# Performance work log

Hardware: AMD Instinct MI355X
Metric: run time of the kernel (lower is better)

Reference implementation:

```python
import jax, jax.numpy as jnp
import numpy as np

# Static config (matches init_kwargs)
B, C, H, W = 8, 256, 128, 128
K = 8            # window size per spatial dim
S = K // 2       # shift size
HEADS = 8
E = 256          # embedding_dim
HEAD_DIM = E // HEADS
HID = 3 * C      # mlp hidden
L = K * K        # tokens per window
NW = (H // K) * (W // K)  # windows per image
EPS = 1e-5


def _shift_mask_np():
    # Standard Swin shifted-window attention mask: True = masked.
    img = np.zeros((H, W), dtype=np.int32)
    cnt = 0
    for hs in (slice(0, -K), slice(-K, -S), slice(-S, None)):
        for ws in (slice(0, -K), slice(-K, -S), slice(-S, None)):
            img[hs, ws] = cnt
            cnt += 1
    ids = img.reshape(H // K, K, W // K, K).transpose(0, 2, 1, 3).reshape(NW, L)
    return ids[:, :, None] != ids[:, None, :]  # (NW, L, L) bool

SHIFT_MASK = jnp.asarray(_shift_mask_np())  # (NW, L, L)


def _rpe_index_np():
    coords = np.stack(np.meshgrid(np.arange(K), np.arange(K), indexing='ij'), -1).reshape(L, 2)
    rel = coords[:, None, :] - coords[None, :, :] + (K - 1)  # (L, L, 2) in [0, 2K-2]
    return rel[..., 0] * (2 * K - 1) + rel[..., 1]  # (L, L)

RPE_IDX = jnp.asarray(_rpe_index_np())  # (L, L) int


def window_partition(x):
    # (B, C, H, W) -> (B, NW, L, C)
    x = x.reshape(B, C, H // K, K, W // K, K)
    return x.transpose(0, 2, 4, 3, 5, 1).reshape(B, NW, L, C)


def window_unpartition(x):
    # (B, NW, L, C) -> (B, C, H, W)
    x = x.reshape(B, H // K, W // K, K, K, C)
    return x.transpose(0, 5, 1, 3, 2, 4).reshape(B, C, H, W)


def layer_norm(x, g, b):
    m = jnp.mean(x, axis=-1, keepdims=True)
    v = jnp.mean(jnp.square(x - m), axis=-1, keepdims=True)
    return (x - m) * jax.lax.rsqrt(v + EPS) * g + b


def setup_inputs() -> dict:
    key = jax.random.key(0)
    ks = jax.random.split(key, 12)
    sc = 0.02
    return {
        'query': jax.random.normal(ks[0], (B, C, H, W), jnp.float32),
        'w_q': jax.random.normal(ks[1], (E, C), jnp.float32) * sc,
        'b_q': jnp.zeros((E,), jnp.float32),
        'w_k': jax.random.normal(ks[2], (E, C), jnp.float32) * sc,
        'b_k': jnp.zeros((E,), jnp.float32),
        'w_v': jax.random.normal(ks[3], (E, C), jnp.float32) * sc,
        'b_v': jnp.zeros((E,), jnp.float32),
        'w_proj': jax.random.normal(ks[4], (C, E), jnp.float32) * sc,
        'b_proj': jnp.zeros((C,), jnp.float32),
        'gamma_attn': jnp.ones((C,), jnp.float32),
        'beta_attn': jnp.zeros((C,), jnp.float32),
        'w1': jax.random.normal(ks[5], (HID, C), jnp.float32) * sc,
        'b1': jnp.zeros((HID,), jnp.float32),
        'w2': jax.random.normal(ks[6], (C, HID), jnp.float32) * sc,
        'b2': jnp.zeros((C,), jnp.float32),
        'gamma_mlp': jnp.ones((C,), jnp.float32),
        'beta_mlp': jnp.zeros((C,), jnp.float32),
        'rpe_table': jax.random.normal(ks[7], ((2 * K - 1) ** 2, HEADS), jnp.float32) * sc,
    }


def reference(query, w_q, b_q, w_k, b_k, w_v, b_v, w_proj, b_proj,
              gamma_attn, beta_attn, w1, b1, w2, b2, gamma_mlp, beta_mlp,
              rpe_table) -> jnp.ndarray:
    # cyclic shift (shifted=True)
    xs = jnp.roll(query, (-S, -S), axis=(2, 3))
    xw = window_partition(xs)  # (B, NW, L, C)

    # windowed multi-head attention with relative positional bias
    q = (jnp.einsum('bwlc,ec->bwle', xw, w_q) + b_q).reshape(B, NW, L, HEADS, HEAD_DIM)
    k = (jnp.einsum('bwlc,ec->bwle', xw, w_k) + b_k).reshape(B, NW, L, HEADS, HEAD_DIM)
    v = (jnp.einsum('bwlc,ec->bwle', xw, w_v) + b_v).reshape(B, NW, L, HEADS, HEAD_DIM)
    scale = HEAD_DIM ** -0.5
    scores = jnp.einsum('bwqhd,bwkhd->bwhqk', q, k) * scale  # (B, NW, H, L, L)
    bias = rpe_table[RPE_IDX].transpose(2, 0, 1)  # (HEADS, L, L)
    scores = scores + bias
    scores = jnp.where(SHIFT_MASK[None, :, None, :, :], jnp.float32(-1e9), scores)
    attn = jax.nn.softmax(scores, axis=-1)
    ctx = jnp.einsum('bwhqk,bwkhd->bwqhd', attn, v).reshape(B, NW, L, E)
    attn_out = jnp.einsum('bwle,ce->bwlc', ctx, w_proj) + b_proj

    # post-attention norm + residual (dropout/droppath inactive in eval)
    x = layer_norm(attn_out, gamma_attn, beta_attn) + xw

    # MLP (GELU) + norm + residual
    h = jax.nn.gelu(jnp.einsum('bwlc,hc->bwlh', x, w1) + b1)
    mlp_out = jnp.einsum('bwlh,ch->bwlc', h, w2) + b2
    x = layer_norm(mlp_out, gamma_mlp, beta_mlp) + x

    out = window_unpartition(x)  # (B, C, H, W)
    return jnp.roll(out, (S, S), axis=(2, 3))
```

## Files before the change

### kernel.cpp

```cpp
#include <hip/hip_runtime.h>
#include <hip/hip_bf16.h>

typedef __attribute__((ext_vector_type(8))) __bf16 bf16x8;
typedef __attribute__((ext_vector_type(4))) float f32x4;
typedef __hip_bfloat16 bf16_t;

#define MFMA(a, b, c) __builtin_amdgcn_mfma_f32_16x16x32_bf16((a), (b), (c), 0, 0, 0)

constexpr int XS = 264;
constexpr int CS = 72;
constexpr int XBYTES = 64 * XS * 2;
constexpr int QC_OFF = XBYTES;
constexpr int KC_OFF = QC_OFF + 64 * CS * 2;
constexpr int VC_OFF = KC_OFF + 64 * CS * 2;
constexpr int SCR_OFF = XBYTES + XBYTES;
constexpr int RPE_OFF = SCR_OFF + 64 * 8 * 4;
constexpr int SMEM_TOTAL = RPE_OFF + 225 * 8 * 4;

constexpr size_t O_WQ = 0;
constexpr size_t O_BQ = O_WQ + 65536;
constexpr size_t O_WK = O_BQ + 256;
constexpr size_t O_BK = O_WK + 65536;
constexpr size_t O_WV = O_BK + 256;
constexpr size_t O_BV = O_WV + 65536;
constexpr size_t O_WP = O_BV + 256;
constexpr size_t O_BP = O_WP + 65536;
constexpr size_t O_GA = O_BP + 256;
constexpr size_t O_BA = O_GA + 256;
constexpr size_t O_W1 = O_BA + 256;
constexpr size_t O_B1 = O_W1 + 196608;
constexpr size_t O_W2 = O_B1 + 768;
constexpr size_t O_B2 = O_W2 + 196608;
constexpr size_t O_GM = O_B2 + 256;
constexpr size_t O_BM = O_GM + 256;
constexpr size_t O_RPE = O_BM + 256;
constexpr size_t W_TOTAL = O_RPE + 1800;

__device__ __forceinline__ float red16(float v) {
    v += __shfl_xor(v, 1);
    v += __shfl_xor(v, 2);
    v += __shfl_xor(v, 4);
    v += __shfl_xor(v, 8);
    return v;
}
__device__ __forceinline__ unsigned short bfbits(float x) {
    bf16_t b = __float2bfloat16(x);
    unsigned short u;
    __builtin_memcpy(&u, &b, 2);
    return u;
}
__device__ __forceinline__ ushort4 pack4(float a, float b, float c, float d) {
    ushort4 u;
    u.x = bfbits(a); u.y = bfbits(b); u.z = bfbits(c); u.w = bfbits(d);
    return u;
}

template <typename T>
__device__ __forceinline__ bf16x8 ldfrag(const T* p) {
    if constexpr (sizeof(T) == 4) {
        const float4* q = reinterpret_cast<const float4*>(p);
        float4 a = q[0], b = q[1];
        bf16x8 r;
        r[0] = static_cast<__bf16>(a.x); r[1] = static_cast<__bf16>(a.y);
        r[2] = static_cast<__bf16>(a.z); r[3] = static_cast<__bf16>(a.w);
        r[4] = static_cast<__bf16>(b.x); r[5] = static_cast<__bf16>(b.y);
        r[6] = static_cast<__bf16>(b.z); r[7] = static_cast<__bf16>(b.w);
        return r;
    } else {
        return *reinterpret_cast<const bf16x8*>(p);
    }
}
template <typename T>
__device__ __forceinline__ float ld1(const T* p) {
    if constexpr (sizeof(T) == 4) return *reinterpret_cast<const float*>(p);
    else return __bfloat162float(*reinterpret_cast<const bf16_t*>(p));
}

template <typename T, typename WT>
__device__ void swin_body(
    const T* __restrict__ qin,
    const WT* __restrict__ wq, const WT* __restrict__ bq,
    const WT* __restrict__ wk, const WT* __restrict__ bk,
    const WT* __restrict__ wv, const WT* __restrict__ bv,
    const WT* __restrict__ wp, const WT* __restrict__ bp,
    const WT* __restrict__ ga, const WT* __restrict__ ba,
    const WT* __restrict__ w1, const WT* __restrict__ b1,
    const WT* __restrict__ w2, const WT* __restrict__ b2,
    const WT* __restrict__ gm, const WT* __restrict__ bm,
    const WT* __restrict__ rpe,
    float* __restrict__ outp, char* sm)
{
    bf16_t* xb = reinterpret_cast<bf16_t*>(sm);
    unsigned short* xbs = reinterpret_cast<unsigned short*>(sm);
    bf16_t* qcp = reinterpret_cast<bf16_t*>(sm + QC_OFF);
    bf16_t* kcp = reinterpret_cast<bf16_t*>(sm + KC_OFF);
    bf16_t* vcp = reinterpret_cast<bf16_t*>(sm + VC_OFF);
    float*  scr = reinterpret_cast<float*>(sm + SCR_OFF);
    float*  rpl = reinterpret_cast<float*>(sm + RPE_OFF);
    bf16_t* hb  = reinterpret_cast<bf16_t*>(sm + XBYTES);

    const int tid  = threadIdx.x;
    const int wave = tid >> 6;
    const int lane = tid & 63;
    const int quad = lane >> 4;
    const int l15  = lane & 15;
    const int h32  = (wave & 1) * 32;
    const int rw   = (wave >> 1) * 32;
    const int colbase = wave * 64;

    const int sw = ((blockIdx.x & 7) << 8) | (blockIdx.x >> 3);
    const int bi = sw >> 8;
    const int wl = sw & 255;
    const int wh = wl >> 4, ww = wl & 15;

    const T* qbase = qin + (size_t)bi * (256 * 128 * 128);

    for (int u = tid; u < 4096; u += 256) {
        int ch = u >> 4, r = (u >> 1) & 7, hf = u & 1;
        int hs = (wh * 8 + r + 4) & 127;
        int ws = (ww * 8 + hf * 4 + 4) & 127;
        int t0 = r * 8 + hf * 4;
        if constexpr (sizeof(T) == 4) {
            float4 px = *reinterpret_cast<const float4*>(
                reinterpret_cast<const float*>(qbase) + ch * 16384 + hs * 128 + ws);
            xb[(t0 + 0) * XS + ch] = __float2bfloat16(px.x);
            xb[(t0 + 1) * XS + ch] = __float2bfloat16(px.y);
            xb[(t0 + 2) * XS + ch] = __float2bfloat16(px.z);
            xb[(t0 + 3) * XS + ch] = __float2bfloat16(px.w);
        } else {
            ushort4 px = *reinterpret_cast<const ushort4*>(
                reinterpret_cast<const unsigned short*>(qbase) + ch * 16384 + hs * 128 + ws);
            xbs[(t0 + 0) * XS + ch] = px.x;
            xbs[(t0 + 1) * XS + ch] = px.y;
            xbs[(t0 + 2) * XS + ch] = px.z;
            xbs[(t0 + 3) * XS + ch] = px.w;
        }
    }
    for (int u = tid; u < 1800; u += 256)
        rpl[(u & 7) * 225 + (u >> 3)] = ld1(rpe + u);
    __syncthreads();

    const f32x4 zero = {0.f, 0.f, 0.f, 0.f};

    const bool wh15 = (wh == 15), ww15 = (ww == 15);
    int ridx_[2][4][4];
    unsigned int msk_bits = 0;
    for (int mt = 0; mt < 2; ++mt) {
        int qt = rw + mt * 16 + l15;
        int qr = qt >> 3, qc = qt & 7;
        int qid = (wh15 ? (qr < 4 ? 1 : 2) : 0) * 3 + (ww15 ? (qc < 4 ? 1 : 2) : 0);
        for (int nt = 0; nt < 4; ++nt)
            for (int i = 0; i < 4; ++i) {
                int kt = nt * 16 + quad * 4 + i;
                int kr = kt >> 3, kc = kt & 7;
                int kid = (wh15 ? (kr < 4 ? 1 : 2) : 0) * 3 + (ww15 ? (kc < 4 ? 1 : 2) : 0);
                ridx_[mt][nt][i] = (qr - kr + 7) * 15 + (qc - kc + 7);
                if (qid != kid) msk_bits |= 1u << (mt * 16 + nt * 4 + i);
            }
    }

    f32x4 pacc[4][4];
    for (int mt = 0; mt < 4; ++mt) for (int nt = 0; nt < 4; ++nt) pacc[mt][nt] = zero;

    #pragma unroll 1
    for (int p = 0; p < 4; ++p) {
        const int ecb = p * 64;

        bf16x8 wpa[2][4];
        for (int kbi = 0; kbi < 2; ++kbi)
            for (int nt = 0; nt < 4; ++nt)
                wpa[kbi][nt] = ldfrag<WT>(
                    wp + (size_t)(colbase + nt * 16 + l15) * 256 + ecb + kbi * 32 + quad * 8);

        {
            f32x4 qa[4], ka[4], va[4];
            for (int mt = 0; mt < 4; ++mt) { qa[mt] = zero; ka[mt] = zero; va[mt] = zero; }
            const size_t wrow = (size_t)(ecb + wave * 16 + l15) * 256;
            bf16x8 bqf = ldfrag<WT>(wq + wrow + quad * 8);
            bf16x8 bkf = ldfrag<WT>(wk + wrow + quad * 8);
            bf16x8 bvf = ldfrag<WT>(wv + wrow + quad * 8);
            #pragma unroll
            for (int kb = 0; kb < 256; kb += 32) {
                const int kbn = (kb + 32) & 255;
                bf16x8 nqf = ldfrag<WT>(wq + wrow + kbn + quad * 8);
                bf16x8 nkf = ldfrag<WT>(wk + wrow + kbn + quad * 8);
                bf16x8 nvf = ldfrag<WT>(wv + wrow + kbn + quad * 8);
                bf16x8 xf[4];
                for (int mt = 0; mt < 4; ++mt)
                    xf[mt] = *reinterpret_cast<const bf16x8*>(
                        xb + (mt * 16 + l15) * XS + kb + quad * 8);
                __builtin_amdgcn_s_setprio(1);
                for (int mt = 0; mt < 4; ++mt) {
                    qa[mt] = MFMA(bqf, xf[mt], qa[mt]);
                    ka[mt] = MFMA(bkf, xf[mt], ka[mt]);
                    va[mt] = MFMA(xf[mt], bvf, va[mt]);
                }
                __builtin_amdgcn_s_setprio(0);
                bqf = nqf; bkf = nkf; bvf = nvf;
            }
            float bq4[4], bk4[4];
            for (int i = 0; i < 4; ++i) {
                bq4[i] = ld1(bq + ecb + wave * 16 + quad * 4 + i);
                bk4[i] = ld1(bk + ecb + wave * 16 + quad * 4 + i);
            }
            float bbv = ld1(bv + ecb + wave * 16 + l15);
            const float SC = 0.17677669529663687f;
            for (int mt = 0; mt < 4; ++mt) {
                *reinterpret_cast<ushort4*>(qcp + (mt * 16 + l15) * CS + wave * 16 + quad * 4) =
                    pack4((qa[mt][0] + bq4[0]) * SC, (qa[mt][1] + bq4[1]) * SC,
                          (qa[mt][2] + bq4[2]) * SC, (qa[mt][3] + bq4[3]) * SC);
                *reinterpret_cast<ushort4*>(kcp + (mt * 16 + l15) * CS + wave * 16 + quad * 4) =
                    pack4(ka[mt][0] + bk4[0], ka[mt][1] + bk4[1],
                          ka[mt][2] + bk4[2], ka[mt][3] + bk4[3]);
                *reinterpret_cast<ushort4*>(vcp + (wave * 16 + l15) * CS + mt * 16 + quad * 4) =
                    pack4(va[mt][0] + bbv, va[mt][1] + bbv,
                          va[mt][2] + bbv, va[mt][3] + bbv);
            }
        }
        __syncthreads();

        f32x4 sacc[2][4];
        {
            bf16x8 bf_q[2], af_k[4];
            for (int mt = 0; mt < 2; ++mt)
                bf_q[mt] = *reinterpret_cast<const bf16x8*>(
                    qcp + (rw + mt * 16 + l15) * CS + h32 + quad * 8);
            for (int nt = 0; nt < 4; ++nt)
                af_k[nt] = *reinterpret_cast<const bf16x8*>(
                    kcp + (nt * 16 + l15) * CS + h32 + quad * 8);
            __builtin_amdgcn_s_setprio(1);
            for (int mt = 0; mt < 2; ++mt)
                for (int nt = 0; nt < 4; ++nt)
                    sacc[mt][nt] = MFMA(af_k[nt], bf_q[mt], zero);
            __builtin_amdgcn_s_setprio(0);
        }
        __syncthreads();

        const float* rph = rpl + (2 * p + (wave & 1)) * 225;
        bf16_t* preg = (wave & 1) ? kcp : qcp;
        for (int mt = 0; mt < 2; ++mt) {
            for (int nt = 0; nt < 4; ++nt)
                for (int i = 0; i < 4; ++i) {
                    float s = sacc[mt][nt][i];
                    s += rph[ridx_[mt][nt][i]];
                    if (msk_bits & (1u << (mt * 16 + nt * 4 + i))) s = -1e9f;
                    sacc[mt][nt][i] = s;
                }
            float m = sacc[mt][0][0];
            for (int nt = 0; nt < 4; ++nt)
                for (int i = 0; i < 4; ++i) m = fmaxf(m, sacc[mt][nt][i]);
            m = fmaxf(m, __shfl_xor(m, 16));
            m = fmaxf(m, __shfl_xor(m, 32));
            float ssum = 0.f;
            for (int nt = 0; nt < 4; ++nt)
                for (int i = 0; i < 4; ++i) {
                    float e = __expf(sacc[mt][nt][i] - m);
                    sacc[mt][nt][i] = e;
                    ssum += e;
                }
            ssum += __shfl_xor(ssum, 16);
            ssum += __shfl_xor(ssum, 32);
            float inv = 1.0f / ssum;
            for (int nt = 0; nt < 4; ++nt)
                *reinterpret_cast<ushort4*>(
                    preg + (rw + mt * 16 + l15) * CS + nt * 16 + quad * 4) =
                    pack4(sacc[mt][nt][0] * inv, sacc[mt][nt][1] * inv,
                          sacc[mt][nt][2] * inv, sacc[mt][nt][3] * inv);
        }

        f32x4 cacc[2][2];
        for (int mt = 0; mt < 2; ++mt) for (int n2 = 0; n2 < 2; ++n2) cacc[mt][n2] = zero;
        for (int kb = 0; kb < 64; kb += 32) {
            bf16x8 bf_p[2], af_v[2];
            for (int mt = 0; mt < 2; ++mt)
                bf_p[mt] = *reinterpret_cast<const bf16x8*>(
                    preg + (rw + mt * 16 + l15) * CS + kb + quad * 8);
            for (int n2 = 0; n2 < 2; ++n2)
                af_v[n2] = *reinterpret_cast<const bf16x8*>(
                    vcp + (h32 + n2 * 16 + l15) * CS + kb + quad * 8);
            __builtin_amdgcn_s_setprio(1);
            for (int mt = 0; mt < 2; ++mt)
                for (int n2 = 0; n2 < 2; ++n2)
                    cacc[mt][n2] = MFMA(af_v[n2], bf_p[mt], cacc[mt][n2]);
            __builtin_amdgcn_s_setprio(0);
        }
        for (int mt = 0; mt < 2; ++mt)
            for (int n2 = 0; n2 < 2; ++n2)
                *reinterpret_cast<ushort4*>(
                    preg + (rw + mt * 16 + l15) * CS + n2 * 16 + quad * 4) =
                    pack4(cacc[mt][n2][0], cacc[mt][n2][1],
                          cacc[mt][n2][2], cacc[mt][n2][3]);
        __syncthreads();

        for (int kbi = 0; kbi < 2; ++kbi) {
            const bf16_t* creg = kbi ? kcp : qcp;
            bf16x8 af[4];
            for (int mt = 0; mt < 4; ++mt)
                af[mt] = *reinterpret_cast<const bf16x8*>(
                    creg + (mt * 16 + l15) * CS + quad * 8);
            __builtin_amdgcn_s_setprio(1);
            for (int mt = 0; mt < 4; ++mt)
                for (int nt = 0; nt < 4; ++nt)
                    pacc[mt][nt] = MFMA(af[mt], wpa[kbi][nt], pacc[mt][nt]);
            __builtin_amdgcn_s_setprio(0);
        }
        __syncthreads();
    }

    auto layernorm_resid = [&](f32x4 (&acc)[4][4], const WT* gamma, const WT* beta) {
        for (int mt = 0; mt < 4; ++mt)
            for (int rg = 0; rg < 4; ++rg) {
                float s = 0.f, sq = 0.f;
                for (int nt = 0; nt < 4; ++nt) {
                    float v = acc[mt][nt][rg];
                    s += v;
                    sq += v * v;
                }
                s = red16(s);
                sq = red16(sq);
                if (l15 == 0) {
                    int tok = mt * 16 + quad * 4 + rg;
                    scr[tok * 8 + wave * 2 + 0] = s;
                    scr[tok * 8 + wave * 2 + 1] = sq;
                }
            }
        __syncthreads();
        for (int mt = 0; mt < 4; ++mt)
            for (int rg = 0; rg < 4; ++rg) {
                int tok = mt * 16 + quad * 4 + rg;
                float S = 0.f, SQ = 0.f;
                for (int w_ = 0; w_ < 4; ++w_) {
                    S += scr[tok * 8 + w_ * 2 + 0];
                    SQ += scr[tok * 8 + w_ * 2 + 1];
                }
                float mean = S * (1.f / 256.f);
                float var = fmaxf(SQ * (1.f / 256.f) - mean * mean, 0.f);
                float rstd = rsqrtf(var + 1e-5f);
                for (int nt = 0; nt < 4; ++nt) {
                    int c = colbase + nt * 16 + l15;
                    float g = ld1(gamma + c);
                    float b_ = ld1(beta + c);
                    float res = __bfloat162float(xb[tok * XS + c]);
                    float o = (acc[mt][nt][rg] - mean) * rstd * g + b_ + res;
                    xb[tok * XS + c] = __float2bfloat16(o);
                }
            }
        __syncthreads();
    };

    {
        for (int nt = 0; nt < 4; ++nt) {
            float bb = ld1(bp + colbase + nt * 16 + l15);
            for (int mt = 0; mt < 4; ++mt)
                for (int rg = 0; rg < 4; ++rg) pacc[mt][nt][rg] += bb;
        }
        layernorm_resid(pacc, ga, ba);
    }

    {
        f32x4 oacc[4][4];
        for (int mt = 0; mt < 4; ++mt) for (int nt = 0; nt < 4; ++nt) oacc[mt][nt] = zero;
        for (int hc = 0; hc < 3; ++hc) {
            f32x4 hacc[4][4];
            for (int nt = 0; nt < 4; ++nt) for (int mt = 0; mt < 4; ++mt) hacc[nt][mt] = zero;
            {
                bf16x8 wf[4], nwf[4];
                for (int nt = 0; nt < 4; ++nt)
                    wf[nt] = ldfrag<WT>(
                        w1 + (size_t)(hc * 256 + colbase + nt * 16 + l15) * 256 + quad * 8);
                #pragma unroll
                for (int kb = 0; kb < 256; kb += 32) {
                    const int kbn = (kb + 32) & 255;
                    for (int nt = 0; nt < 4; ++nt)
                        nwf[nt] = ldfrag<WT>(
                            w1 + (size_t)(hc * 256 + colbase + nt * 16 + l15) * 256 + kbn + quad * 8);
                    bf16x8 xf[4];
                    for (int mt = 0; mt < 4; ++mt)
                        xf[mt] = *reinterpret_cast<const bf16x8*>(
                            xb + (mt * 16 + l15) * XS + kb + quad * 8);
                    __builtin_amdgcn_s_setprio(1);
                    for (int nt = 0; nt < 4; ++nt)
                        for (int mt = 0; mt < 4; ++mt)
                            hacc[nt][mt] = MFMA(wf[nt], xf[mt], hacc[nt][mt]);
                    __builtin_amdgcn_s_setprio(0);
                    for (int nt = 0; nt < 4; ++nt) wf[nt] = nwf[nt];
                }
            }
            for (int nt = 0; nt < 4; ++nt) {
                float b4[4];
                for (int i = 0; i < 4; ++i)
                    b4[i] = ld1(b1 + hc * 256 + colbase + nt * 16 + quad * 4 + i);
                for (int mt = 0; mt < 4; ++mt) {
                    float g4[4];
                    for (int i = 0; i < 4; ++i) {
                        float x = hacc[nt][mt][i] + b4[i];
                        float u = 0.7978845608f * (x + 0.044715f * x * x * x);
                        float t = 1.f - 2.f / (1.f + __expf(2.f * u));
                        g4[i] = 0.5f * x * (1.f + t);
                    }
                    *reinterpret_cast<ushort4*>(
                        hb + (mt * 16 + l15) * XS + colbase + nt * 16 + quad * 4) =
                        pack4(g4[0], g4[1], g4[2], g4[3]);
                }
            }
            __syncthreads();
            {
                bf16x8 bfr[4], nbfr[4];
                for (int nt = 0; nt < 4; ++nt)
                    bfr[nt] = ldfrag<WT>(
                        w2 + (size_t)(colbase + nt * 16 + l15) * 768 + hc * 256 + quad * 8);
                #pragma unroll
                for (int kb = 0; kb < 256; kb += 32) {
                    const int kbn = (kb + 32) & 255;
                    for (int nt = 0; nt < 4; ++nt)
                        nbfr[nt] = ldfrag<WT>(
                            w2 + (size_t)(colbase + nt * 16 + l15) * 768 + hc * 256 + kbn + quad * 8);
                    bf16x8 af[4];
                    for (int mt = 0; mt < 4; ++mt)
                        af[mt] = *reinterpret_cast<const bf16x8*>(
                            hb + (mt * 16 + l15) * XS + kb + quad * 8);
                    __builtin_amdgcn_s_setprio(1);
                    for (int mt = 0; mt < 4; ++mt)
                        for (int nt = 0; nt < 4; ++nt)
                            oacc[mt][nt] = MFMA(af[mt], bfr[nt], oacc[mt][nt]);
                    __builtin_amdgcn_s_setprio(0);
                    for (int nt = 0; nt < 4; ++nt) bfr[nt] = nbfr[nt];
                }
            }
            __syncthreads();
        }
        for (int nt = 0; nt < 4; ++nt) {
            float bb = ld1(b2 + colbase + nt * 16 + l15);
            for (int mt = 0; mt < 4; ++mt)
                for (int rg = 0; rg < 4; ++rg) oacc[mt][nt][rg] += bb;
        }
        layernorm_resid(oacc, gm, bm);
    }

    for (int u = tid; u < 4096; u += 256) {
        int ch = u >> 4, r = (u >> 1) & 7, hf = u & 1;
        int hs = (wh * 8 + r + 4) & 127;
        int ws = (ww * 8 + hf * 4 + 4) & 127;
        int t0 = r * 8 + hf * 4;
        float4 px;
        px.x = __bfloat162float(xb[(t0 + 0) * XS + ch]);
        px.y = __bfloat162float(xb[(t0 + 1) * XS + ch]);
        px.z = __bfloat162float(xb[(t0 + 2) * XS + ch]);
        px.w = __bfloat162float(xb[(t0 + 3) * XS + ch]);
        *reinterpret_cast<float4*>(
            outp + (size_t)bi * 4194304 + ch * 16384 + hs * 128 + ws) = px;
    }
}

__global__ void convert_weights_kernel(
    const void* wq, const void* bq, const void* wk, const void* bk,
    const void* wv, const void* bv, const void* wp, const void* bp,
    const void* ga, const void* ba, const void* w1, const void* b1,
    const void* w2, const void* b2, const void* gm, const void* bm,
    const void* rpe, bf16_t* ws)
{
    if (*reinterpret_cast<const unsigned short*>(ga) == 0x3F80) return;
    const float* srcs[17] = {
        (const float*)wq, (const float*)bq, (const float*)wk, (const float*)bk,
        (const float*)wv, (const float*)bv, (const float*)wp, (const float*)bp,
        (const float*)ga, (const float*)ba, (const float*)w1, (const float*)b1,
        (const float*)w2, (const float*)b2, (const float*)gm, (const float*)bm,
        (const float*)rpe};
    const size_t offs[18] = {O_WQ, O_BQ, O_WK, O_BK, O_WV, O_BV, O_WP, O_BP, O_GA,
                             O_BA, O_W1, O_B1, O_W2, O_B2, O_GM, O_BM, O_RPE, W_TOTAL};
    for (size_t i = blockIdx.x * (size_t)blockDim.x + threadIdx.x; i < W_TOTAL;
         i += (size_t)gridDim.x * blockDim.x) {
        int s = 0;
        while (s < 16 && i >= offs[s + 1]) ++s;
        ws[i] = __float2bfloat16(srcs[s][i - offs[s]]);
    }
}

__global__ __launch_bounds__(256, 2) void swin_block_kernel(
    const void* qin,
    const void* wq, const void* bq, const void* wk, const void* bk,
    const void* wv, const void* bv, const void* wp, const void* bp,
    const void* ga, const void* ba, const void* w1, const void* b1,
    const void* w2, const void* b2, const void* gm, const void* bm,
    const void* rpe, float* outp, const bf16_t* ws, int use_ws)
{
    extern __shared__ char smem[];
    const bool is_bf16 = (*reinterpret_cast<const unsigned short*>(ga) == 0x3F80);
    if (is_bf16) {
        swin_body<bf16_t, bf16_t>((const bf16_t*)qin,
            (const bf16_t*)wq, (const bf16_t*)bq, (const bf16_t*)wk, (const bf16_t*)bk,
            (const bf16_t*)wv, (const bf16_t*)bv, (const bf16_t*)wp, (const bf16_t*)bp,
            (const bf16_t*)ga, (const bf16_t*)ba, (const bf16_t*)w1, (const bf16_t*)b1,
            (const bf16_t*)w2, (const bf16_t*)b2, (const bf16_t*)gm, (const bf16_t*)bm,
            (const bf16_t*)rpe, outp, smem);
    } else if (use_ws) {
        swin_body<float, bf16_t>((const float*)qin,
            ws + O_WQ, ws + O_BQ, ws + O_WK, ws + O_BK, ws + O_WV, ws + O_BV,
            ws + O_WP, ws + O_BP, ws + O_GA, ws + O_BA, ws + O_W1, ws + O_B1,
            ws + O_W2, ws + O_B2, ws + O_GM, ws + O_BM, ws + O_RPE, outp, smem);
    } else {
        swin_body<float, float>((const float*)qin,
            (const float*)wq, (const float*)bq, (const float*)wk, (const float*)bk,
            (const float*)wv, (const float*)bv, (const float*)wp, (const float*)bp,
            (const float*)ga, (const float*)ba, (const float*)w1, (const float*)b1,
            (const float*)w2, (const float*)b2, (const float*)gm, (const float*)bm,
            (const float*)rpe, outp, smem);
    }
}

extern "C" void kernel_launch(void* const* d_in, const int* in_sizes, int n_in,
                              void* d_out, int out_size, void* d_ws, size_t ws_size,
                              hipStream_t stream) {
    (void)in_sizes; (void)n_in; (void)out_size;
    const int use_ws = (d_ws != nullptr && ws_size >= W_TOTAL * sizeof(bf16_t)) ? 1 : 0;
    if (use_ws) {
        convert_weights_kernel<<<256, 256, 0, stream>>>(
            d_in[1], d_in[2], d_in[3], d_in[4], d_in[5], d_in[6], d_in[7], d_in[8],
            d_in[9], d_in[10], d_in[11], d_in[12], d_in[13], d_in[14], d_in[15], d_in[16],
            d_in[17], (bf16_t*)d_ws);
    }
    hipFuncSetAttribute(reinterpret_cast<const void*>(swin_block_kernel),
                        hipFuncAttributeMaxDynamicSharedMemorySize, SMEM_TOTAL);
    swin_block_kernel<<<2048, 256, SMEM_TOTAL, stream>>>(
        d_in[0], d_in[1], d_in[2], d_in[3], d_in[4], d_in[5], d_in[6], d_in[7], d_in[8],
        d_in[9], d_in[10], d_in[11], d_in[12], d_in[13], d_in[14], d_in[15], d_in[16],
        d_in[17], (float*)d_out, (const bf16_t*)d_ws, use_ws);
}
```

Measured before the change: 789.5 us.

## Assign one attention head per wave with register-resident Q and probabilities

Restructures the attention so each wave owns a full head (32 dims) over all 64 tokens, processing two head groups instead of four 64-wide chunks. Q and softmax probabilities stay in registers and are redistributed into MFMA B-fragments with lane shuffles, which removes their LDS round-trips and most of the per-chunk block barriers. The output projection is deferred to a single pass over all 256 context dims. RPE bias is now read from global memory (transposed in the workspace) instead of being staged in LDS. The tradeoff is higher register pressure from the large accumulator arrays and extra shuffles, plus scattered global bias loads.

Result: slower. 909.7 us (+15.2%).

```diff
diff --git a/kernel.cpp b/kernel.cpp
--- a/kernel.cpp
+++ b/kernel.cpp
@@ -3,19 +3,19 @@
 
 typedef __attribute__((ext_vector_type(8))) __bf16 bf16x8;
 typedef __attribute__((ext_vector_type(4))) float f32x4;
+typedef __attribute__((ext_vector_type(4))) unsigned int u32x4;
 typedef __hip_bfloat16 bf16_t;
 
 #define MFMA(a, b, c) __builtin_amdgcn_mfma_f32_16x16x32_bf16((a), (b), (c), 0, 0, 0)
 
 constexpr int XS = 264;
-constexpr int CS = 72;
+constexpr int CS = 136;
+constexpr int VS = 72;
 constexpr int XBYTES = 64 * XS * 2;
-constexpr int QC_OFF = XBYTES;
-constexpr int KC_OFF = QC_OFF + 64 * CS * 2;
-constexpr int VC_OFF = KC_OFF + 64 * CS * 2;
-constexpr int SCR_OFF = XBYTES + XBYTES;
-constexpr int RPE_OFF = SCR_OFF + 64 * 8 * 4;
-constexpr int SMEM_TOTAL = RPE_OFF + 225 * 8 * 4;
+constexpr int KC_OFF = XBYTES;
+constexpr int VT_OFF = KC_OFF + 64 * CS * 2;
+constexpr int SCR_OFF = VT_OFF + 128 * VS * 2;
+constexpr int SMEM_TOTAL = SCR_OFF + 64 * 8 * 4;
 
 constexpr size_t O_WQ = 0;
 constexpr size_t O_BQ = O_WQ + 65536;
@@ -54,6 +54,9 @@
     u.x = bfbits(a); u.y = bfbits(b); u.z = bfbits(c); u.w = bfbits(d);
     return u;
 }
+__device__ __forceinline__ unsigned pack2(float lo, float hi) {
+    return (unsigned)bfbits(lo) | ((unsigned)bfbits(hi) << 16);
+}
 
 template <typename T>
 __device__ __forceinline__ bf16x8 ldfrag(const T* p) {
@@ -87,25 +90,21 @@
     const WT* __restrict__ w1, const WT* __restrict__ b1,
     const WT* __restrict__ w2, const WT* __restrict__ b2,
     const WT* __restrict__ gm, const WT* __restrict__ bm,
-    const WT* __restrict__ rpe,
+    const WT* __restrict__ rpe, int rpe_sh, int rpe_sr,
     float* __restrict__ outp, char* sm)
 {
-    bf16_t* xb = reinterpret_cast<bf16_t*>(sm);
+    bf16_t* xb  = reinterpret_cast<bf16_t*>(sm);
     unsigned short* xbs = reinterpret_cast<unsigned short*>(sm);
-    bf16_t* qcp = reinterpret_cast<bf16_t*>(sm + QC_OFF);
     bf16_t* kcp = reinterpret_cast<bf16_t*>(sm + KC_OFF);
-    bf16_t* vcp = reinterpret_cast<bf16_t*>(sm + VC_OFF);
+    bf16_t* vtp = reinterpret_cast<bf16_t*>(sm + VT_OFF);
+    bf16_t* hb  = reinterpret_cast<bf16_t*>(sm + KC_OFF);
     float*  scr = reinterpret_cast<float*>(sm + SCR_OFF);
-    float*  rpl = reinterpret_cast<float*>(sm + RPE_OFF);
-    bf16_t* hb  = reinterpret_cast<bf16_t*>(sm + XBYTES);
 
     const int tid  = threadIdx.x;
     const int wave = tid >> 6;
     const int lane = tid & 63;
     const int quad = lane >> 4;
     const int l15  = lane & 15;
-    const int h32  = (wave & 1) * 32;
-    const int rw   = (wave >> 1) * 32;
     const int colbase = wave * 64;
 
     const int sw = ((blockIdx.x & 7) << 8) | (blockIdx.x >> 3);
@@ -136,17 +135,14 @@
             xbs[(t0 + 3) * XS + ch] = px.w;
         }
     }
-    for (int u = tid; u < 1800; u += 256)
-        rpl[(u & 7) * 225 + (u >> 3)] = ld1(rpe + u);
     __syncthreads();
 
     const f32x4 zero = {0.f, 0.f, 0.f, 0.f};
 
     const bool wh15 = (wh == 15), ww15 = (ww == 15);
-    int ridx_[2][4][4];
-    unsigned int msk_bits = 0;
-    for (int mt = 0; mt < 2; ++mt) {
-        int qt = rw + mt * 16 + l15;
+    unsigned long long msk64 = 0ull;
+    for (int mtB = 0; mtB < 4; ++mtB) {
+        int qt = mtB * 16 + l15;
         int qr = qt >> 3, qc = qt & 7;
         int qid = (wh15 ? (qr < 4 ? 1 : 2) : 0) * 3 + (ww15 ? (qc < 4 ? 1 : 2) : 0);
         for (int nt = 0; nt < 4; ++nt)
@@ -154,157 +150,219 @@
                 int kt = nt * 16 + quad * 4 + i;
                 int kr = kt >> 3, kc = kt & 7;
                 int kid = (wh15 ? (kr < 4 ? 1 : 2) : 0) * 3 + (ww15 ? (kc < 4 ? 1 : 2) : 0);
-                ridx_[mt][nt][i] = (qr - kr + 7) * 15 + (qc - kc + 7);
-                if (qid != kid) msk_bits |= 1u << (mt * 16 + nt * 4 + i);
-            }
-    }
-
-    f32x4 pacc[4][4];
-    for (int mt = 0; mt < 4; ++mt) for (int nt = 0; nt < 4; ++nt) pacc[mt][nt] = zero;
-
+                if (qid != kid) msk64 |= 1ull << (mtB * 16 + nt * 4 + i);
+            }
+    }
+
+    auto mkbf = [&](const unsigned* w, int lostep, int kbase) -> bf16x8 {
+        u32x4 r;
+        #pragma unroll
+        for (int t = 0; t < 4; ++t) {
+            int srcl = (quad & 1) * 32 + (t >> 1) * 16 + l15;
+            unsigned lo = (unsigned)__shfl((int)w[(kbase >> 3) + (t & 1)], srcl);
+            unsigned hi = (unsigned)__shfl((int)w[(kbase >> 3) + lostep + (t & 1)], srcl);
+            r[t] = (quad & 2) ? hi : lo;
+        }
+        return __builtin_bit_cast(bf16x8, r);
+    };
+
+    const float SC = 0.17677669529663687f;
+
+    f32x4 cacc[4][2];
+    uint2 cw1[4][2];
     #pragma unroll 1
-    for (int p = 0; p < 4; ++p) {
-        const int ecb = p * 64;
-
-        bf16x8 wpa[2][4];
-        for (int kbi = 0; kbi < 2; ++kbi)
-            for (int nt = 0; nt < 4; ++nt)
-                wpa[kbi][nt] = ldfrag<WT>(
-                    wp + (size_t)(colbase + nt * 16 + l15) * 256 + ecb + kbi * 32 + quad * 8);
-
+    for (int p = 0; p < 2; ++p) {
+        const int ew = p * 128 + wave * 32;
+
+        unsigned qq[16];
         {
-            f32x4 qa[4], ka[4], va[4];
-            for (int mt = 0; mt < 4; ++mt) { qa[mt] = zero; ka[mt] = zero; va[mt] = zero; }
-            const size_t wrow = (size_t)(ecb + wave * 16 + l15) * 256;
-            bf16x8 bqf = ldfrag<WT>(wq + wrow + quad * 8);
-            bf16x8 bkf = ldfrag<WT>(wk + wrow + quad * 8);
-            bf16x8 bvf = ldfrag<WT>(wv + wrow + quad * 8);
-            #pragma unroll
+            f32x4 qa[2][4];
+            for (int et = 0; et < 2; ++et) for (int mt = 0; mt < 4; ++mt) qa[et][mt] = zero;
             for (int kb = 0; kb < 256; kb += 32) {
-                const int kbn = (kb + 32) & 255;
-                bf16x8 nqf = ldfrag<WT>(wq + wrow + kbn + quad * 8);
-                bf16x8 nkf = ldfrag<WT>(wk + wrow + kbn + quad * 8);
-                bf16x8 nvf = ldfrag<WT>(wv + wrow + kbn + quad * 8);
-                bf16x8 xf[4];
+                bf16x8 xf[4], wf[2];
                 for (int mt = 0; mt < 4; ++mt)
                     xf[mt] = *reinterpret_cast<const bf16x8*>(
                         xb + (mt * 16 + l15) * XS + kb + quad * 8);
+                for (int et = 0; et < 2; ++et)
+                    wf[et] = ldfrag<WT>(wq + (size_t)(ew + et * 16 + l15) * 256 + kb + quad * 8);
                 __builtin_amdgcn_s_setprio(1);
+                for (int et = 0; et < 2; ++et)
+                    for (int mt = 0; mt < 4; ++mt)
+                        qa[et][mt] = MFMA(wf[et], xf[mt], qa[et][mt]);
+                __builtin_amdgcn_s_setprio(0);
+            }
+            for (int et = 0; et < 2; ++et) {
+                float b4[4];
+                for (int i = 0; i < 4; ++i)
+                    b4[i] = ld1(bq + ew + et * 16 + quad * 4 + i);
                 for (int mt = 0; mt < 4; ++mt) {
-                    qa[mt] = MFMA(bqf, xf[mt], qa[mt]);
-                    ka[mt] = MFMA(bkf, xf[mt], ka[mt]);
-                    va[mt] = MFMA(xf[mt], bvf, va[mt]);
-                }
+                    qq[et * 8 + mt * 2 + 0] = pack2((qa[et][mt][0] + b4[0]) * SC,
+                                                    (qa[et][mt][1] + b4[1]) * SC);
+                    qq[et * 8 + mt * 2 + 1] = pack2((qa[et][mt][2] + b4[2]) * SC,
+                                                    (qa[et][mt][3] + b4[3]) * SC);
+                }
+            }
+        }
+
+        {
+            f32x4 ka[2][4];
+            for (int et = 0; et < 2; ++et) for (int mt = 0; mt < 4; ++mt) ka[et][mt] = zero;
+            for (int kb = 0; kb < 256; kb += 32) {
+                bf16x8 xf[4], wf[2];
+                for (int mt = 0; mt < 4; ++mt)
+                    xf[mt] = *reinterpret_cast<const bf16x8*>(
+                        xb + (mt * 16 + l15) * XS + kb + quad * 8);
+                for (int et = 0; et < 2; ++et)
+                    wf[et] = ldfrag<WT>(wk + (size_t)(ew + et * 16 + l15) * 256 + kb + quad * 8);
+                __builtin_amdgcn_s_setprio(1);
+                for (int et = 0; et < 2; ++et)
+                    for (int mt = 0; mt < 4; ++mt)
+                        ka[et][mt] = MFMA(wf[et], xf[mt], ka[et][mt]);
                 __builtin_amdgcn_s_setprio(0);
-                bqf = nqf; bkf = nkf; bvf = nvf;
-            }
-            float bq4[4], bk4[4];
-            for (int i = 0; i < 4; ++i) {
-                bq4[i] = ld1(bq + ecb + wave * 16 + quad * 4 + i);
-                bk4[i] = ld1(bk + ecb + wave * 16 + quad * 4 + i);
-            }
-            float bbv = ld1(bv + ecb + wave * 16 + l15);
-            const float SC = 0.17677669529663687f;
-            for (int mt = 0; mt < 4; ++mt) {
-                *reinterpret_cast<ushort4*>(qcp + (mt * 16 + l15) * CS + wave * 16 + quad * 4) =
-                    pack4((qa[mt][0] + bq4[0]) * SC, (qa[mt][1] + bq4[1]) * SC,
-                          (qa[mt][2] + bq4[2]) * SC, (qa[mt][3] + bq4[3]) * SC);
-                *reinterpret_cast<ushort4*>(kcp + (mt * 16 + l15) * CS + wave * 16 + quad * 4) =
-                    pack4(ka[mt][0] + bk4[0], ka[mt][1] + bk4[1],
-                          ka[mt][2] + bk4[2], ka[mt][3] + bk4[3]);
-                *reinterpret_cast<ushort4*>(vcp + (wave * 16 + l15) * CS + mt * 16 + quad * 4) =
-                    pack4(va[mt][0] + bbv, va[mt][1] + bbv,
-                          va[mt][2] + bbv, va[mt][3] + bbv);
-            }
-        }
-        __syncthreads();
-
-        f32x4 sacc[2][4];
+            }
+            for (int et = 0; et < 2; ++et) {
+                float b4[4];
+                for (int i = 0; i < 4; ++i)
+                    b4[i] = ld1(bk + ew + et * 16 + quad * 4 + i);
+                for (int mt = 0; mt < 4; ++mt)
+                    *reinterpret_cast<ushort4*>(
+                        kcp + (mt * 16 + l15) * CS + wave * 32 + et * 16 + quad * 4) =
+                        pack4(ka[et][mt][0] + b4[0], ka[et][mt][1] + b4[1],
+                              ka[et][mt][2] + b4[2], ka[et][mt][3] + b4[3]);
+            }
+        }
+
+        f32x4 sacc[4][4];
         {
-            bf16x8 bf_q[2], af_k[4];
-            for (int mt = 0; mt < 2; ++mt)
-                bf_q[mt] = *reinterpret_cast<const bf16x8*>(
-                    qcp + (rw + mt * 16 + l15) * CS + h32 + quad * 8);
+            bf16x8 af_k[4];
             for (int nt = 0; nt < 4; ++nt)
                 af_k[nt] = *reinterpret_cast<const bf16x8*>(
-                    kcp + (nt * 16 + l15) * CS + h32 + quad * 8);
+                    kcp + (nt * 16 + l15) * CS + wave * 32 + quad * 8);
             __builtin_amdgcn_s_setprio(1);
-            for (int mt = 0; mt < 2; ++mt)
+            #pragma unroll
+            for (int mtB = 0; mtB < 4; ++mtB) {
+                bf16x8 bq_ = mkbf(qq + mtB * 2, 8, 0);
                 for (int nt = 0; nt < 4; ++nt)
-                    sacc[mt][nt] = MFMA(af_k[nt], bf_q[mt], zero);
+                    sacc[mtB][nt] = MFMA(af_k[nt], bq_, zero);
+            }
             __builtin_amdgcn_s_setprio(0);
         }
-        __syncthreads();
-
-        const float* rph = rpl + (2 * p + (wave & 1)) * 225;
-        bf16_t* preg = (wave & 1) ? kcp : qcp;
-        for (int mt = 0; mt < 2; ++mt) {
+
+        const WT* rph = rpe + (size_t)(p * 4 + wave) * rpe_sh;
+        unsigned pw[4][8];
+        #pragma unroll
+        for (int mtB = 0; mtB < 4; ++mtB) {
+            int qt = mtB * 16 + l15;
+            int qr = qt >> 3, qc = qt & 7;
             for (int nt = 0; nt < 4; ++nt)
                 for (int i = 0; i < 4; ++i) {
-                    float s = sacc[mt][nt][i];
-                    s += rph[ridx_[mt][nt][i]];
-                    if (msk_bits & (1u << (mt * 16 + nt * 4 + i))) s = -1e9f;
-                    sacc[mt][nt][i] = s;
-                }
-            float m = sacc[mt][0][0];
+                    int kt = nt * 16 + quad * 4 + i;
+                    int ridx = (qr - (kt >> 3) + 7) * 15 + (qc - (kt & 7) + 7);
+                    float s = sacc[mtB][nt][i] + ld1(rph + (size_t)ridx * rpe_sr);
+                    if ((msk64 >> (mtB * 16 + nt * 4 + i)) & 1) s = -1e9f;
+                    sacc[mtB][nt][i] = s;
+                }
+            float m = sacc[mtB][0][0];
             for (int nt = 0; nt < 4; ++nt)
-                for (int i = 0; i < 4; ++i) m = fmaxf(m, sacc[mt][nt][i]);
+                for (int i = 0; i < 4; ++i) m = fmaxf(m, sacc[mtB][nt][i]);
             m = fmaxf(m, __shfl_xor(m, 16));
             m = fmaxf(m, __shfl_xor(m, 32));
             float ssum = 0.f;
             for (int nt = 0; nt < 4; ++nt)
                 for (int i = 0; i < 4; ++i) {
-                    float e = __expf(sacc[mt][nt][i] - m);
-                    sacc[mt][nt][i] = e;
+                    float e = __expf(sacc[mtB][nt][i] - m);
+                    sacc[mtB][nt][i] = e;
                     ssum += e;
                 }
             ssum += __shfl_xor(ssum, 16);
             ssum += __shfl_xor(ssum, 32);
             float inv = 1.0f / ssum;
             for (int nt = 0; nt < 4; ++nt)
-                *reinterpret_cast<ushort4*>(
-                    preg + (rw + mt * 16 + l15) * CS + nt * 16 + quad * 4) =
-                    pack4(sacc[mt][nt][0] * inv, sacc[mt][nt][1] * inv,
-                          sacc[mt][nt][2] * inv, sacc[mt][nt][3] * inv);
-        }
-
-        f32x4 cacc[2][2];
-        for (int mt = 0; mt < 2; ++mt) for (int n2 = 0; n2 < 2; ++n2) cacc[mt][n2] = zero;
+                for (int h2 = 0; h2 < 2; ++h2)
+                    pw[mtB][nt * 2 + h2] = pack2(sacc[mtB][nt][2 * h2] * inv,
+                                                 sacc[mtB][nt][2 * h2 + 1] * inv);
+        }
+
+        {
+            f32x4 va[2][4];
+            for (int et = 0; et < 2; ++et) for (int mt = 0; mt < 4; ++mt) va[et][mt] = zero;
+            for (int kb = 0; kb < 256; kb += 32) {
+                bf16x8 xf[4], wf[2];
+                for (int mt = 0; mt < 4; ++mt)
+                    xf[mt] = *reinterpret_cast<const bf16x8*>(
+                        xb + (mt * 16 + l15) * XS + kb + quad * 8);
+                for (int et = 0; et < 2; ++et)
+                    wf[et] = ldfrag<WT>(wv + (size_t)(ew + et * 16 + l15) * 256 + kb + quad * 8);
+                __builtin_amdgcn_s_setprio(1);
+                for (int et = 0; et < 2; ++et)
+                    for (int mt = 0; mt < 4; ++mt)
+                        va[et][mt] = MFMA(xf[mt], wf[et], va[et][mt]);
+                __builtin_amdgcn_s_setprio(0);
+            }
+            for (int et = 0; et < 2; ++et) {
+                float bbv = ld1(bv + ew + et * 16 + l15);
+                for (int mt = 0; mt < 4; ++mt)
+                    *reinterpret_cast<ushort4*>(
+                        vtp + (wave * 32 + et * 16 + l15) * VS + mt * 16 + quad * 4) =
+                        pack4(va[et][mt][0] + bbv, va[et][mt][1] + bbv,
+                              va[et][mt][2] + bbv, va[et][mt][3] + bbv);
+            }
+        }
+
+        for (int mtB = 0; mtB < 4; ++mtB)
+            for (int n2 = 0; n2 < 2; ++n2) cacc[mtB][n2] = zero;
         for (int kb = 0; kb < 64; kb += 32) {
-            bf16x8 bf_p[2], af_v[2];
-            for (int mt = 0; mt < 2; ++mt)
-                bf_p[mt] = *reinterpret_cast<const bf16x8*>(
-                    preg + (rw + mt * 16 + l15) * CS + kb + quad * 8);
+            bf16x8 af_v[2];
             for (int n2 = 0; n2 < 2; ++n2)
                 af_v[n2] = *reinterpret_cast<const bf16x8*>(
-                    vcp + (h32 + n2 * 16 + l15) * CS + kb + quad * 8);
+                    vtp + (wave * 32 + n2 * 16 + l15) * VS + kb + quad * 8);
             __builtin_amdgcn_s_setprio(1);
-            for (int mt = 0; mt < 2; ++mt)
+            #pragma unroll
+            for (int mtB = 0; mtB < 4; ++mtB) {
+                bf16x8 bp_ = mkbf(pw[mtB], 2, kb);
                 for (int n2 = 0; n2 < 2; ++n2)
-                    cacc[mt][n2] = MFMA(af_v[n2], bf_p[mt], cacc[mt][n2]);
+                    cacc[mtB][n2] = MFMA(af_v[n2], bp_, cacc[mtB][n2]);
+            }
             __builtin_amdgcn_s_setprio(0);
         }
-        for (int mt = 0; mt < 2; ++mt)
-            for (int n2 = 0; n2 < 2; ++n2)
-                *reinterpret_cast<ushort4*>(
-                    preg + (rw + mt * 16 + l15) * CS + n2 * 16 + quad * 4) =
-                    pack4(cacc[mt][n2][0], cacc[mt][n2][1],
-                          cacc[mt][n2][2], cacc[mt][n2][3]);
-        __syncthreads();
-
-        for (int kbi = 0; kbi < 2; ++kbi) {
-            const bf16_t* creg = kbi ? kcp : qcp;
-            bf16x8 af[4];
-            for (int mt = 0; mt < 4; ++mt)
-                af[mt] = *reinterpret_cast<const bf16x8*>(
-                    creg + (mt * 16 + l15) * CS + quad * 8);
-            __builtin_amdgcn_s_setprio(1);
-            for (int mt = 0; mt < 4; ++mt)
-                for (int nt = 0; nt < 4; ++nt)
-                    pacc[mt][nt] = MFMA(af[mt], wpa[kbi][nt], pacc[mt][nt]);
-            __builtin_amdgcn_s_setprio(0);
-        }
-        __syncthreads();
+        if (p == 0) {
+            for (int mtB = 0; mtB < 4; ++mtB)
+                for (int n2 = 0; n2 < 2; ++n2) {
+                    cw1[mtB][n2].x = pack2(cacc[mtB][n2][0], cacc[mtB][n2][1]);
+                    cw1[mtB][n2].y = pack2(cacc[mtB][n2][2], cacc[mtB][n2][3]);
+                }
+        }
+    }
+    __syncthreads();
+
+    for (int mtB = 0; mtB < 4; ++mtB)
+        for (int n2 = 0; n2 < 2; ++n2) {
+            *reinterpret_cast<uint2*>(
+                vtp + (mtB * 16 + l15) * CS + wave * 32 + n2 * 16 + quad * 4) = cw1[mtB][n2];
+            *reinterpret_cast<ushort4*>(
+                kcp + (mtB * 16 + l15) * CS + wave * 32 + n2 * 16 + quad * 4) =
+                pack4(cacc[mtB][n2][0], cacc[mtB][n2][1],
+                      cacc[mtB][n2][2], cacc[mtB][n2][3]);
+        }
+    __syncthreads();
+
+    f32x4 pacc[4][4];
+    for (int mt = 0; mt < 4; ++mt) for (int nt = 0; nt < 4; ++nt) pacc[mt][nt] = zero;
+    #pragma unroll
+    for (int kbi = 0; kbi < 8; ++kbi) {
+        const bf16_t* creg = (kbi < 4) ? vtp : kcp;
+        const int kl = (kbi & 3) * 32;
+        bf16x8 af[4], bfr[4];
+        for (int mt = 0; mt < 4; ++mt)
+            af[mt] = *reinterpret_cast<const bf16x8*>(
+                creg + (mt * 16 + l15) * CS + kl + quad * 8);
+        for (int nt = 0; nt < 4; ++nt)
+            bfr[nt] = ldfrag<WT>(wp + (size_t)(colbase + nt * 16 + l15) * 256 + kbi * 32 + quad * 8);
+        __builtin_amdgcn_s_setprio(1);
+        for (int mt = 0; mt < 4; ++mt)
+            for (int nt = 0; nt < 4; ++nt)
+                pacc[mt][nt] = MFMA(af[mt], bfr[nt], pacc[mt][nt]);
+        __builtin_amdgcn_s_setprio(0);
     }
 
     auto layernorm_resid = [&](f32x4 (&acc)[4][4], const WT* gamma, const WT* beta) {
@@ -472,7 +530,13 @@
          i += (size_t)gridDim.x * blockDim.x) {
         int s = 0;
         while (s < 16 && i >= offs[s + 1]) ++s;
-        ws[i] = __float2bfloat16(srcs[s][i - offs[s]]);
+        bf16_t v = __float2bfloat16(srcs[s][i - offs[s]]);
+        if (s == 16) {
+            size_t local = i - O_RPE;
+            ws[O_RPE + (local & 7) * 225 + (local >> 3)] = v;
+        } else {
+            ws[i] = v;
+        }
     }
 }
 
@@ -492,19 +556,19 @@
             (const bf16_t*)wv, (const bf16_t*)bv, (const bf16_t*)wp, (const bf16_t*)bp,
             (const bf16_t*)ga, (const bf16_t*)ba, (const bf16_t*)w1, (const bf16_t*)b1,
             (const bf16_t*)w2, (const bf16_t*)b2, (const bf16_t*)gm, (const bf16_t*)bm,
-            (const bf16_t*)rpe, outp, smem);
+            (const bf16_t*)rpe, 1, 8, outp, smem);
     } else if (use_ws) {
         swin_body<float, bf16_t>((const float*)qin,
             ws + O_WQ, ws + O_BQ, ws + O_WK, ws + O_BK, ws + O_WV, ws + O_BV,
             ws + O_WP, ws + O_BP, ws + O_GA, ws + O_BA, ws + O_W1, ws + O_B1,
-            ws + O_W2, ws + O_B2, ws + O_GM, ws + O_BM, ws + O_RPE, outp, smem);
+            ws + O_W2, ws + O_B2, ws + O_GM, ws + O_BM, ws + O_RPE, 225, 1, outp, smem);
     } else {
         swin_body<float, float>((const float*)qin,
             (const float*)wq, (const float*)bq, (const float*)wk, (const float*)bk,
             (const float*)wv, (const float*)bv, (const float*)wp, (const float*)bp,
             (const float*)ga, (const float*)ba, (const float*)w1, (const float*)b1,
             (const float*)w2, (const float*)b2, (const float*)gm, (const float*)bm,
-            (const float*)rpe, outp, smem);
+            (const float*)rpe, 1, 8, outp, smem);
     }
 }
 
```
